# Kernel optimization log

Hardware: AMD Instinct MI355X
Metric: run time of the kernel (lower is better)

Reference implementation:

```python
import jax, jax.numpy as jnp
import numpy as np

G, K, N, T = 16, 2048, 2048, 16384  # groups, in_features, out_features, total_tokens


def setup_inputs() -> dict:
    key = jax.random.key(0)
    k1, k2 = jax.random.split(key)
    hidden_states = jax.random.normal(k1, (T, K), dtype=jnp.float32)
    # kaiming_uniform_(a=sqrt(5)) on [G, K, N] -> bound = sqrt(6 / ((1 + 5) * fan_in)) = 1/sqrt(K)
    bound = 1.0 / np.sqrt(K)
    weight = jax.random.uniform(k2, (G, K, N), dtype=jnp.float32, minval=-bound, maxval=bound)
    tokens_per_group = T // G
    tokens_per_expert = jnp.full((G,), tokens_per_group, dtype=jnp.int32)
    # offsets[0] = 0, offsets[i] = start of group i (matches _group_sizes_from_offsets)
    offsets = jnp.arange(G, dtype=jnp.int32) * tokens_per_group
    blockscale_offsets = offsets  # unused by the eager math path; carried for signature fidelity
    return {
        "hidden_states": hidden_states,
        "weight": weight,
        "offsets": offsets,
        "blockscale_offsets": blockscale_offsets,
        "tokens_per_expert": tokens_per_expert,
    }


def reference(hidden_states, weight, offsets, blockscale_offsets, tokens_per_expert):
    # Grouped (ragged) GEMM: rows [offsets[g] : offsets[g]+tokens_per_expert[g]] of
    # hidden_states are multiplied by weight[g] ([K, N]). tokens_per_expert equals the
    # group sizes derived from offsets in the torch module's eager fallback.
    # jax.lax.ragged_dot is the exact grouped-mm primitive (no dense [T,K,N] gather).
    return jax.lax.ragged_dot(hidden_states, weight, tokens_per_expert)
```

## Files before the change

kernel.cpp:

```cpp
#include <hip/hip_runtime.h>
#include <cstdint>
#include <cstddef>

#define GRP 16
#define KD  2048
#define ND  2048
#define TD  16384

#define BM 128
#define BN 128
#define BK 64

typedef __bf16 bf16x8 __attribute__((ext_vector_type(8)));
typedef float  f32x4  __attribute__((ext_vector_type(4)));

__device__ __forceinline__ uint16_t f2bf(float f) {
  uint32_t u = __builtin_bit_cast(uint32_t, f);
  u += 0x7fffu + ((u >> 16) & 1u);
  return (uint16_t)(u >> 16);
}

__device__ __forceinline__ void gload16(const void* g, void* l) {
  __builtin_amdgcn_global_load_lds((__attribute__((address_space(1))) void*)g,
                                   (__attribute__((address_space(3))) void*)l,
                                   16, 0, 0);
}

__device__ __forceinline__ int find_group(const int* tokens, int row0) {
  int g = GRP - 1, start = 0;
  for (int i = 0; i < GRP; ++i) {
    int sz = tokens[i];
    if (row0 < start + sz) { g = i; break; }
    start += sz;
  }
  return g;
}

__global__ __launch_bounds__(256) void h2bf_kernel(const float* __restrict__ in,
                                                   uint16_t* __restrict__ out) {
  const size_t idx = ((size_t)blockIdx.x * 256 + threadIdx.x) * 8;
  const float4 a = *(const float4*)(in + idx);
  const float4 b = *(const float4*)(in + idx + 4);
  uint4 p;
  p.x = (uint32_t)f2bf(a.x) | ((uint32_t)f2bf(a.y) << 16);
  p.y = (uint32_t)f2bf(a.z) | ((uint32_t)f2bf(a.w) << 16);
  p.z = (uint32_t)f2bf(b.x) | ((uint32_t)f2bf(b.y) << 16);
  p.w = (uint32_t)f2bf(b.z) | ((uint32_t)f2bf(b.w) << 16);
  *(uint4*)(out + idx) = p;
}

__global__ __launch_bounds__(256) void wtrans_kernel(const float* __restrict__ w,
                                                     uint16_t* __restrict__ wT) {
  __shared__ uint32_t tile[64][33];
  const int g  = blockIdx.z;
  const int n0 = blockIdx.x * 64;
  const int k0 = blockIdx.y * 64;
  const float* src = w + (size_t)g * KD * ND;
  uint16_t* dst = wT + (size_t)g * ND * KD;
  const int t = threadIdx.x;

  {
    const int k2 = t >> 4;
    const int n4 = (t & 15) * 4;
    for (int half = 0; half < 2; ++half) {
      const int kp = half * 16 + k2;
      const int k  = kp * 2;
      const float4 v0 = *(const float4*)(src + (size_t)(k0 + k)     * ND + n0 + n4);
      const float4 v1 = *(const float4*)(src + (size_t)(k0 + k + 1) * ND + n0 + n4);
      tile[n4 + 0][kp] = (uint32_t)f2bf(v0.x) | ((uint32_t)f2bf(v1.x) << 16);
      tile[n4 + 1][kp] = (uint32_t)f2bf(v0.y) | ((uint32_t)f2bf(v1.y) << 16);
      tile[n4 + 2][kp] = (uint32_t)f2bf(v0.z) | ((uint32_t)f2bf(v1.z) << 16);
      tile[n4 + 3][kp] = (uint32_t)f2bf(v0.w) | ((uint32_t)f2bf(v1.w) << 16);
    }
  }
  __syncthreads();
  {
    const int n  = t >> 2;
    const int kq = (t & 3) * 8;
    const uint4 a = *(const uint4*)&tile[n][kq];
    const uint4 b = *(const uint4*)&tile[n][kq + 4];
    uint32_t* o = (uint32_t*)(dst + (size_t)(n0 + n) * KD + k0) + kq;
    *(uint4*)(o + 0) = a;
    *(uint4*)(o + 4) = b;
  }
}

__global__ __launch_bounds__(256) void gemm_kernel(const uint16_t* __restrict__ A,
                                                   const uint16_t* __restrict__ Bt,
                                                   const int* __restrict__ tokens,
                                                   float* __restrict__ C) {
  __shared__ uint16_t Alds[BM * BK];
  __shared__ uint16_t Blds[BN * BK];

  const int t    = threadIdx.x;
  const int n0   = blockIdx.x * BN;
  const int row0 = blockIdx.y * BM;

  const int g = find_group(tokens, row0);
  const uint16_t* Bg = Bt + (size_t)g * ND * KD;

  const int lane = t & 63;
  const int wid  = t >> 6;
  const int wm   = wid & 1;
  const int wn   = wid >> 1;
  const int l16  = lane & 15;
  const int quad = lane >> 4;

  f32x4 acc[4][4] = {};

  const uint16_t* Apt[4]; const uint16_t* Bpt[4];
  uint16_t *Al[4], *Bl[4];
  for (int i = 0; i < 4; ++i) {
    const int c = t + 256 * i;
    const int r = c >> 3;
    const int ko = ((c & 7) ^ (r & 7)) * 8;
    Apt[i] = A  + (size_t)(row0 + r) * KD + ko;
    Bpt[i] = Bg + (size_t)(n0  + r) * KD + ko;
    Al[i] = &Alds[c * 8];
    Bl[i] = &Blds[c * 8];
  }

  int aoff[2][4], boff[2][4];
  for (int h = 0; h < 2; ++h) {
    for (int mi = 0; mi < 4; ++mi) {
      const int r = wm * 64 + mi * 16 + l16;
      aoff[h][mi] = r * BK + (((h * 4 + quad) ^ (r & 7)) * 8);
    }
    for (int ni = 0; ni < 4; ++ni) {
      const int r = wn * 64 + ni * 16 + l16;
      boff[h][ni] = r * BK + (((h * 4 + quad) ^ (r & 7)) * 8);
    }
  }

  for (int k0 = 0; k0 < KD; k0 += BK) {
    __syncthreads();
    for (int i = 0; i < 4; ++i) gload16(Apt[i] + k0, Al[i]);
    for (int i = 0; i < 4; ++i) gload16(Bpt[i] + k0, Bl[i]);
    __syncthreads();

    for (int h = 0; h < 2; ++h) {
      bf16x8 af[4], bfr[4];
      for (int mi = 0; mi < 4; ++mi) af[mi]  = *(const bf16x8*)&Alds[aoff[h][mi]];
      for (int ni = 0; ni < 4; ++ni) bfr[ni] = *(const bf16x8*)&Blds[boff[h][ni]];
      for (int mi = 0; mi < 4; ++mi)
        for (int ni = 0; ni < 4; ++ni)
          acc[mi][ni] = __builtin_amdgcn_mfma_f32_16x16x32_bf16(af[mi], bfr[ni],
                                                                acc[mi][ni], 0, 0, 0);
    }
  }

  for (int mi = 0; mi < 4; ++mi) {
    const int m = row0 + wm * 64 + mi * 16 + quad * 4;
    for (int ni = 0; ni < 4; ++ni) {
      const int n = n0 + wn * 64 + ni * 16 + l16;
      for (int r = 0; r < 4; ++r)
        C[(size_t)(m + r) * ND + n] = acc[mi][ni][r];
    }
  }
}

__global__ __launch_bounds__(256) void fb_gemm(const float* __restrict__ A,
                                               const float* __restrict__ W,
                                               const int* __restrict__ tokens,
                                               float* __restrict__ C) {
  __shared__ float As[16][64];
  __shared__ float Bs[16][65];
  const int n0 = blockIdx.x * 64;
  const int m0 = blockIdx.y * 64;
  const int g = find_group(tokens, m0);
  const float* Wg = W + (size_t)g * KD * ND;
  const int tx = threadIdx.x & 15, ty = threadIdx.x >> 4;
  float acc[4][4] = {};
  for (int k0 = 0; k0 < KD; k0 += 16) {
    for (int e = threadIdx.x; e < 64 * 16; e += 256) {
      int m = e >> 4, k = e & 15;
      As[k][m] = A[(size_t)(m0 + m) * KD + k0 + k];
    }
    for (int e = threadIdx.x; e < 64 * 16; e += 256) {
      int n = e & 63, k = e >> 6;
      Bs[k][n] = Wg[(size_t)(k0 + k) * ND + n0 + n];
    }
    __syncthreads();
    for (int k = 0; k < 16; ++k)
      for (int i = 0; i < 4; ++i)
        for (int j = 0; j < 4; ++j)
          acc[i][j] += As[k][ty * 4 + i] * Bs[k][tx * 4 + j];
    __syncthreads();
  }
  for (int i = 0; i < 4; ++i)
    for (int j = 0; j < 4; ++j)
      C[(size_t)(m0 + ty * 4 + i) * ND + n0 + tx * 4 + j] = acc[i][j];
}

extern "C" void kernel_launch(void* const* d_in, const int* in_sizes, int n_in,
                              void* d_out, int out_size, void* d_ws, size_t ws_size,
                              hipStream_t stream) {
  const float* hidden = (const float*)d_in[0];
  const float* weight = (const float*)d_in[1];
  const int*   tokens = (const int*)d_in[4];
  float* out = (float*)d_out;

  const size_t needA = (size_t)TD * KD * 2;
  const size_t needB = (size_t)GRP * ND * KD * 2;

  if (ws_size >= needA + needB) {
    uint16_t* hB = (uint16_t*)d_ws;
    uint16_t* wT = (uint16_t*)((char*)d_ws + needA);
    h2bf_kernel<<<(int)(((size_t)TD * KD) / (256 * 8)), 256, 0, stream>>>(hidden, hB);
    wtrans_kernel<<<dim3(ND / 64, KD / 64, GRP), 256, 0, stream>>>(weight, wT);
    gemm_kernel<<<dim3(ND / BN, TD / BM), 256, 0, stream>>>(hB, wT, tokens, out);
  } else {
    fb_gemm<<<dim3(ND / 64, TD / 64), 256, 0, stream>>>(hidden, weight, tokens, out);
  }
}
```

Baseline: 673.9 us.

## Fuse fp32-to-bf16 conversion and weight transpose into register-prefetched GEMM

Removes the separate conversion and weight-transpose kernels and their workspace round-trip. The GEMM now reads fp32 activations and weights directly, converts them to bf16 in registers, and writes them transposed and swizzled into LDS. The next tile's global loads are issued into registers before the MFMA loop so they overlap with compute. The cost is twice the global bytes per tile, since fp32 inputs are reloaded by every block that uses them, plus strided scalar weight loads and higher register pressure.

```diff
diff --git a/kernel.cpp b/kernel.cpp
--- a/kernel.cpp
+++ b/kernel.cpp
@@ -10,20 +10,17 @@
 #define BM 128
 #define BN 128
 #define BK 64
+#define NT (KD / BK)
 
 typedef __bf16 bf16x8 __attribute__((ext_vector_type(8)));
 typedef float  f32x4  __attribute__((ext_vector_type(4)));
 
-__device__ __forceinline__ uint16_t f2bf(float f) {
-  uint32_t u = __builtin_bit_cast(uint32_t, f);
-  u += 0x7fffu + ((u >> 16) & 1u);
-  return (uint16_t)(u >> 16);
-}
-
-__device__ __forceinline__ void gload16(const void* g, void* l) {
-  __builtin_amdgcn_global_load_lds((__attribute__((address_space(1))) void*)g,
-                                   (__attribute__((address_space(3))) void*)l,
-                                   16, 0, 0);
+__device__ __forceinline__ uint32_t pk2bf(float x, float y) {
+  uint32_t ux = __builtin_bit_cast(uint32_t, x);
+  uint32_t uy = __builtin_bit_cast(uint32_t, y);
+  ux += 0x7fffu + ((ux >> 16) & 1u);
+  uy += 0x7fffu + ((uy >> 16) & 1u);
+  return __builtin_amdgcn_perm(uy, ux, 0x07060302);
 }
 
 __device__ __forceinline__ int find_group(const int* tokens, int row0) {
@@ -36,59 +33,9 @@
   return g;
 }
 
-__global__ __launch_bounds__(256) void h2bf_kernel(const float* __restrict__ in,
-                                                   uint16_t* __restrict__ out) {
-  const size_t idx = ((size_t)blockIdx.x * 256 + threadIdx.x) * 8;
-  const float4 a = *(const float4*)(in + idx);
-  const float4 b = *(const float4*)(in + idx + 4);
-  uint4 p;
-  p.x = (uint32_t)f2bf(a.x) | ((uint32_t)f2bf(a.y) << 16);
-  p.y = (uint32_t)f2bf(a.z) | ((uint32_t)f2bf(a.w) << 16);
-  p.z = (uint32_t)f2bf(b.x) | ((uint32_t)f2bf(b.y) << 16);
-  p.w = (uint32_t)f2bf(b.z) | ((uint32_t)f2bf(b.w) << 16);
-  *(uint4*)(out + idx) = p;
-}
-
-__global__ __launch_bounds__(256) void wtrans_kernel(const float* __restrict__ w,
-                                                     uint16_t* __restrict__ wT) {
-  __shared__ uint32_t tile[64][33];
-  const int g  = blockIdx.z;
-  const int n0 = blockIdx.x * 64;
-  const int k0 = blockIdx.y * 64;
-  const float* src = w + (size_t)g * KD * ND;
-  uint16_t* dst = wT + (size_t)g * ND * KD;
-  const int t = threadIdx.x;
-
-  {
-    const int k2 = t >> 4;
-    const int n4 = (t & 15) * 4;
-    for (int half = 0; half < 2; ++half) {
-      const int kp = half * 16 + k2;
-      const int k  = kp * 2;
-      const float4 v0 = *(const float4*)(src + (size_t)(k0 + k)     * ND + n0 + n4);
-      const float4 v1 = *(const float4*)(src + (size_t)(k0 + k + 1) * ND + n0 + n4);
-      tile[n4 + 0][kp] = (uint32_t)f2bf(v0.x) | ((uint32_t)f2bf(v1.x) << 16);
-      tile[n4 + 1][kp] = (uint32_t)f2bf(v0.y) | ((uint32_t)f2bf(v1.y) << 16);
-      tile[n4 + 2][kp] = (uint32_t)f2bf(v0.z) | ((uint32_t)f2bf(v1.z) << 16);
-      tile[n4 + 3][kp] = (uint32_t)f2bf(v0.w) | ((uint32_t)f2bf(v1.w) << 16);
-    }
-  }
-  __syncthreads();
-  {
-    const int n  = t >> 2;
-    const int kq = (t & 3) * 8;
-    const uint4 a = *(const uint4*)&tile[n][kq];
-    const uint4 b = *(const uint4*)&tile[n][kq + 4];
-    uint32_t* o = (uint32_t*)(dst + (size_t)(n0 + n) * KD + k0) + kq;
-    *(uint4*)(o + 0) = a;
-    *(uint4*)(o + 4) = b;
-  }
-}
-
-__global__ __launch_bounds__(256) void gemm_kernel(const uint16_t* __restrict__ A,
-                                                   const uint16_t* __restrict__ Bt,
-                                                   const int* __restrict__ tokens,
-                                                   float* __restrict__ C) {
+__global__ __launch_bounds__(256, 2)
+void fused_gemm(const float* __restrict__ A, const float* __restrict__ W,
+                const int* __restrict__ tokens, float* __restrict__ C) {
   __shared__ uint16_t Alds[BM * BK];
   __shared__ uint16_t Blds[BN * BK];
 
@@ -97,7 +44,7 @@
   const int row0 = blockIdx.y * BM;
 
   const int g = find_group(tokens, row0);
-  const uint16_t* Bg = Bt + (size_t)g * ND * KD;
+  const float* Wg = W + (size_t)g * KD * ND;
 
   const int lane = t & 63;
   const int wid  = t >> 6;
@@ -106,18 +53,23 @@
   const int l16  = lane & 15;
   const int quad = lane >> 4;
 
-  f32x4 acc[4][4] = {};
+  const float* aptr[4];
+  uint32_t*    adst[4];
+  for (int i = 0; i < 4; ++i) {
+    const int c  = t + 256 * i;
+    const int r  = c >> 3;
+    const int cl = c & 7;
+    aptr[i] = A + (size_t)(row0 + r) * KD + cl * 8;
+    adst[i] = (uint32_t*)&Alds[(r * 8 + (cl ^ (r & 7))) * 8];
+  }
 
-  const uint16_t* Apt[4]; const uint16_t* Bpt[4];
-  uint16_t *Al[4], *Bl[4];
-  for (int i = 0; i < 4; ++i) {
-    const int c = t + 256 * i;
-    const int r = c >> 3;
-    const int ko = ((c & 7) ^ (r & 7)) * 8;
-    Apt[i] = A  + (size_t)(row0 + r) * KD + ko;
-    Bpt[i] = Bg + (size_t)(n0  + r) * KD + ko;
-    Al[i] = &Alds[c * 8];
-    Bl[i] = &Blds[c * 8];
+  const int nl = t & 127;
+  const int bh = t >> 7;
+  const float* bptr = Wg + (size_t)(bh * 32) * ND + n0 + nl;
+  uint32_t* bdst[4];
+  for (int c = 0; c < 4; ++c) {
+    const int kc = bh * 4 + c;
+    bdst[c] = (uint32_t*)&Blds[(nl * 8 + (kc ^ (nl & 7))) * 8];
   }
 
   int aoff[2][4], boff[2][4];
@@ -132,64 +84,80 @@
     }
   }
 
-  for (int k0 = 0; k0 < KD; k0 += BK) {
-    __syncthreads();
-    for (int i = 0; i < 4; ++i) gload16(Apt[i] + k0, Al[i]);
-    for (int i = 0; i < 4; ++i) gload16(Bpt[i] + k0, Bl[i]);
+  f32x4 acc[4][4] = {};
+
+  float4 ar[4][2];
+  float  br[4][8];
+
+  auto issue = [&](int k0) {
+    #pragma unroll
+    for (int i = 0; i < 4; ++i) {
+      ar[i][0] = *(const float4*)(aptr[i] + k0);
+      ar[i][1] = *(const float4*)(aptr[i] + k0 + 4);
+    }
+    const float* bp = bptr + (size_t)k0 * ND;
+    #pragma unroll
+    for (int c = 0; c < 4; ++c)
+      #pragma unroll
+      for (int j = 0; j < 8; ++j)
+        br[c][j] = bp[(size_t)(c * 8 + j) * ND];
+  };
+
+  issue(0);
+
+  for (int kt = 0; kt < NT; ++kt) {
     __syncthreads();
 
+    #pragma unroll
+    for (int i = 0; i < 4; ++i) {
+      uint4 p;
+      p.x = pk2bf(ar[i][0].x, ar[i][0].y);
+      p.y = pk2bf(ar[i][0].z, ar[i][0].w);
+      p.z = pk2bf(ar[i][1].x, ar[i][1].y);
+      p.w = pk2bf(ar[i][1].z, ar[i][1].w);
+      *(uint4*)adst[i] = p;
+    }
+    #pragma unroll
+    for (int c = 0; c < 4; ++c) {
+      uint4 p;
+      p.x = pk2bf(br[c][0], br[c][1]);
+      p.y = pk2bf(br[c][2], br[c][3]);
+      p.z = pk2bf(br[c][4], br[c][5]);
+      p.w = pk2bf(br[c][6], br[c][7]);
+      *(uint4*)bdst[c] = p;
+    }
+
+    if (kt + 1 < NT) issue((kt + 1) * BK);
+
+    __syncthreads();
+
+    #pragma unroll
     for (int h = 0; h < 2; ++h) {
       bf16x8 af[4], bfr[4];
+      #pragma unroll
       for (int mi = 0; mi < 4; ++mi) af[mi]  = *(const bf16x8*)&Alds[aoff[h][mi]];
+      #pragma unroll
       for (int ni = 0; ni < 4; ++ni) bfr[ni] = *(const bf16x8*)&Blds[boff[h][ni]];
+      #pragma unroll
       for (int mi = 0; mi < 4; ++mi)
+        #pragma unroll
         for (int ni = 0; ni < 4; ++ni)
           acc[mi][ni] = __builtin_amdgcn_mfma_f32_16x16x32_bf16(af[mi], bfr[ni],
                                                                 acc[mi][ni], 0, 0, 0);
     }
   }
 
+  #pragma unroll
   for (int mi = 0; mi < 4; ++mi) {
     const int m = row0 + wm * 64 + mi * 16 + quad * 4;
+    #pragma unroll
     for (int ni = 0; ni < 4; ++ni) {
       const int n = n0 + wn * 64 + ni * 16 + l16;
+      #pragma unroll
       for (int r = 0; r < 4; ++r)
         C[(size_t)(m + r) * ND + n] = acc[mi][ni][r];
     }
   }
-}
-
-__global__ __launch_bounds__(256) void fb_gemm(const float* __restrict__ A,
-                                               const float* __restrict__ W,
-                                               const int* __restrict__ tokens,
-                                               float* __restrict__ C) {
-  __shared__ float As[16][64];
-  __shared__ float Bs[16][65];
-  const int n0 = blockIdx.x * 64;
-  const int m0 = blockIdx.y * 64;
-  const int g = find_group(tokens, m0);
-  const float* Wg = W + (size_t)g * KD * ND;
-  const int tx = threadIdx.x & 15, ty = threadIdx.x >> 4;
-  float acc[4][4] = {};
-  for (int k0 = 0; k0 < KD; k0 += 16) {
-    for (int e = threadIdx.x; e < 64 * 16; e += 256) {
-      int m = e >> 4, k = e & 15;
-      As[k][m] = A[(size_t)(m0 + m) * KD + k0 + k];
-    }
-    for (int e = threadIdx.x; e < 64 * 16; e += 256) {
-      int n = e & 63, k = e >> 6;
-      Bs[k][n] = Wg[(size_t)(k0 + k) * ND + n0 + n];
-    }
-    __syncthreads();
-    for (int k = 0; k < 16; ++k)
-      for (int i = 0; i < 4; ++i)
-        for (int j = 0; j < 4; ++j)
-          acc[i][j] += As[k][ty * 4 + i] * Bs[k][tx * 4 + j];
-    __syncthreads();
-  }
-  for (int i = 0; i < 4; ++i)
-    for (int j = 0; j < 4; ++j)
-      C[(size_t)(m0 + ty * 4 + i) * ND + n0 + tx * 4 + j] = acc[i][j];
 }
 
 extern "C" void kernel_launch(void* const* d_in, const int* in_sizes, int n_in,
@@ -199,17 +167,7 @@
   const float* weight = (const float*)d_in[1];
   const int*   tokens = (const int*)d_in[4];
   float* out = (float*)d_out;
+  (void)d_ws; (void)ws_size;
 
-  const size_t needA = (size_t)TD * KD * 2;
-  const size_t needB = (size_t)GRP * ND * KD * 2;
-
-  if (ws_size >= needA + needB) {
-    uint16_t* hB = (uint16_t*)d_ws;
-    uint16_t* wT = (uint16_t*)((char*)d_ws + needA);
-    h2bf_kernel<<<(int)(((size_t)TD * KD) / (256 * 8)), 256, 0, stream>>>(hidden, hB);
-    wtrans_kernel<<<dim3(ND / 64, KD / 64, GRP), 256, 0, stream>>>(weight, wT);
-    gemm_kernel<<<dim3(ND / BN, TD / BM), 256, 0, stream>>>(hB, wT, tokens, out);
-  } else {
-    fb_gemm<<<dim3(ND / 64, TD / 64), 256, 0, stream>>>(hidden, weight, tokens, out);
-  }
+  fused_gemm<<<dim3(ND / BN, TD / BM), 256, 0, stream>>>(hidden, weight, tokens, out);
 }
```

After: 693.9 us. 1.03x slower.

## Rewrite grouped GEMM as 256x256 double-buffered pipelined kernel with block swizzle

Applied to the files above, without the earlier changes.

Replaces the 128x128 single-buffered GEMM with a 256x256 tile, 512-thread kernel that double-buffers A and B tiles in LDS. Global-to-LDS loads for the next K tile are interleaved with MFMA phases, using explicit vmcnt waits, barriers and setprio. Blocks are remapped through a swizzle so neighbouring blocks share weight tiles in L2. It also changes the wtrans store pattern so each wave writes a contiguous run. The cost is heavier register and LDS pressure (8x4 accumulators per thread, 128KB LDS) and fragile hand-written wait counts.

```diff
diff --git a/kernel.cpp b/kernel.cpp
--- a/kernel.cpp
+++ b/kernel.cpp
@@ -7,9 +7,10 @@
 #define ND  2048
 #define TD  16384
 
-#define BM 128
-#define BN 128
+#define BM 256
+#define BN 256
 #define BK 64
+#define NTILE (KD / BK)
 
 typedef __bf16 bf16x8 __attribute__((ext_vector_type(8)));
 typedef float  f32x4  __attribute__((ext_vector_type(4)));
@@ -76,83 +77,134 @@
   __syncthreads();
   {
     const int n  = t >> 2;
-    const int kq = (t & 3) * 8;
+    const int kq = (t & 3) * 4;
     const uint4 a = *(const uint4*)&tile[n][kq];
-    const uint4 b = *(const uint4*)&tile[n][kq + 4];
-    uint32_t* o = (uint32_t*)(dst + (size_t)(n0 + n) * KD + k0) + kq;
-    *(uint4*)(o + 0) = a;
-    *(uint4*)(o + 4) = b;
-  }
-}
-
-__global__ __launch_bounds__(256) void gemm_kernel(const uint16_t* __restrict__ A,
-                                                   const uint16_t* __restrict__ Bt,
-                                                   const int* __restrict__ tokens,
-                                                   float* __restrict__ C) {
-  __shared__ uint16_t Alds[BM * BK];
-  __shared__ uint16_t Blds[BN * BK];
-
-  const int t    = threadIdx.x;
-  const int n0   = blockIdx.x * BN;
-  const int row0 = blockIdx.y * BM;
+    const uint4 b = *(const uint4*)&tile[n][kq + 16];
+    uint32_t* o = (uint32_t*)(dst + (size_t)(n0 + n) * KD + k0);
+    *(uint4*)(o + kq)      = a;
+    *(uint4*)(o + kq + 16) = b;
+  }
+}
+
+__global__ __launch_bounds__(512, 2)
+void gemm_kernel(const uint16_t* __restrict__ A, const uint16_t* __restrict__ Bt,
+                 const int* __restrict__ tokens, float* __restrict__ C) {
+  __shared__ uint16_t Alds[2][2][128 * 64];
+  __shared__ uint16_t Blds[2][2][128 * 64];
+
+  const int t = threadIdx.x;
+  const int bid = blockIdx.x;
+  const int swz = (bid & 7) * 64 + (bid >> 3);
+  const int bx = swz & 7, by = swz >> 3;
+  const int n0 = bx * BN, row0 = by * BM;
 
   const int g = find_group(tokens, row0);
   const uint16_t* Bg = Bt + (size_t)g * ND * KD;
 
-  const int lane = t & 63;
-  const int wid  = t >> 6;
-  const int wm   = wid & 1;
-  const int wn   = wid >> 1;
-  const int l16  = lane & 15;
-  const int quad = lane >> 4;
-
-  f32x4 acc[4][4] = {};
-
-  const uint16_t* Apt[4]; const uint16_t* Bpt[4];
-  uint16_t *Al[4], *Bl[4];
-  for (int i = 0; i < 4; ++i) {
-    const int c = t + 256 * i;
+  const int lane = t & 63, wid = t >> 6;
+  const int wm = wid & 1;
+  const int wn = wid >> 1;
+  const int l16 = lane & 15, quad = lane >> 4;
+
+  const uint16_t* pA[2]; const uint16_t* pB[2];
+  int doff[2];
+  #pragma unroll
+  for (int j = 0; j < 2; ++j) {
+    const int c = t + 512 * j;
     const int r = c >> 3;
     const int ko = ((c & 7) ^ (r & 7)) * 8;
-    Apt[i] = A  + (size_t)(row0 + r) * KD + ko;
-    Bpt[i] = Bg + (size_t)(n0  + r) * KD + ko;
-    Al[i] = &Alds[c * 8];
-    Bl[i] = &Blds[c * 8];
-  }
-
-  int aoff[2][4], boff[2][4];
-  for (int h = 0; h < 2; ++h) {
-    for (int mi = 0; mi < 4; ++mi) {
-      const int r = wm * 64 + mi * 16 + l16;
-      aoff[h][mi] = r * BK + (((h * 4 + quad) ^ (r & 7)) * 8);
-    }
-    for (int ni = 0; ni < 4; ++ni) {
-      const int r = wn * 64 + ni * 16 + l16;
-      boff[h][ni] = r * BK + (((h * 4 + quad) ^ (r & 7)) * 8);
-    }
-  }
-
-  for (int k0 = 0; k0 < KD; k0 += BK) {
-    __syncthreads();
-    for (int i = 0; i < 4; ++i) gload16(Apt[i] + k0, Al[i]);
-    for (int i = 0; i < 4; ++i) gload16(Bpt[i] + k0, Bl[i]);
-    __syncthreads();
-
-    for (int h = 0; h < 2; ++h) {
-      bf16x8 af[4], bfr[4];
-      for (int mi = 0; mi < 4; ++mi) af[mi]  = *(const bf16x8*)&Alds[aoff[h][mi]];
-      for (int ni = 0; ni < 4; ++ni) bfr[ni] = *(const bf16x8*)&Blds[boff[h][ni]];
-      for (int mi = 0; mi < 4; ++mi)
-        for (int ni = 0; ni < 4; ++ni)
-          acc[mi][ni] = __builtin_amdgcn_mfma_f32_16x16x32_bf16(af[mi], bfr[ni],
-                                                                acc[mi][ni], 0, 0, 0);
-    }
-  }
-
-  for (int mi = 0; mi < 4; ++mi) {
-    const int m = row0 + wm * 64 + mi * 16 + quad * 4;
+    pA[j] = A  + (size_t)(row0 + r) * KD + ko;
+    pB[j] = Bg + (size_t)(n0  + r) * KD + ko;
+    doff[j] = c * 8;
+  }
+
+  int arow[8], brow[4], axk[2];
+  #pragma unroll
+  for (int mi = 0; mi < 8; ++mi) arow[mi] = (mi * 16 + l16) * 64;
+  #pragma unroll
+  for (int ni = 0; ni < 4; ++ni) brow[ni] = ((wn & 1) * 64 + ni * 16 + l16) * 64;
+  #pragma unroll
+  for (int kh = 0; kh < 2; ++kh) axk[kh] = ((kh * 4 + quad) ^ (l16 & 7)) * 8;
+
+  const uint16_t* Abase[2] = { &Alds[0][wm][0],      &Alds[1][wm][0] };
+  const uint16_t* Bbase[2] = { &Blds[0][wn >> 1][0], &Blds[1][wn >> 1][0] };
+
+  f32x4 acc[8][4] = {};
+  bf16x8 bfr[2][4];
+
+#define STAGE_A(buf, half, T) do {                                              \
+    gload16(pA[0] + (size_t)(half) * 128 * KD + (T) * BK, &Alds[buf][half][doff[0]]); \
+    gload16(pA[1] + (size_t)(half) * 128 * KD + (T) * BK, &Alds[buf][half][doff[1]]); \
+  } while (0)
+#define STAGE_B(buf, half, T) do {                                              \
+    gload16(pB[0] + (size_t)(half) * 128 * KD + (T) * BK, &Blds[buf][half][doff[0]]); \
+    gload16(pB[1] + (size_t)(half) * 128 * KD + (T) * BK, &Blds[buf][half][doff[1]]); \
+  } while (0)
+#define NOSTAGE do {} while (0)
+#define VM4 asm volatile("s_waitcnt vmcnt(4)" ::: "memory")
+#define VM0 asm volatile("s_waitcnt vmcnt(0)" ::: "memory")
+#define NOWAIT do {} while (0)
+#define LGK0 asm volatile("s_waitcnt lgkmcnt(0)" ::: "memory")
+#define BARRIER do { asm volatile("" ::: "memory");                             \
+    __builtin_amdgcn_s_barrier(); asm volatile("" ::: "memory"); } while (0)
+
+#define PHASE(buf, mib, DO_B, STAGE_STMT, ENDWAIT) do {                         \
+    if (DO_B) {                                                                 \
+      _Pragma("unroll") for (int kh2 = 0; kh2 < 2; ++kh2)                       \
+        _Pragma("unroll") for (int ni2 = 0; ni2 < 4; ++ni2)                     \
+          bfr[kh2][ni2] = *(const bf16x8*)&Bbase[buf][brow[ni2] + axk[kh2]];    \
+    }                                                                           \
+    bf16x8 af[2][2];                                                            \
+    _Pragma("unroll") for (int kh2 = 0; kh2 < 2; ++kh2)                         \
+      _Pragma("unroll") for (int m2 = 0; m2 < 2; ++m2)                          \
+        af[kh2][m2] = *(const bf16x8*)&Abase[buf][arow[(mib) + m2] + axk[kh2]]; \
+    STAGE_STMT;                                                                 \
+    BARRIER;                                                                    \
+    __builtin_amdgcn_s_setprio(1);                                              \
+    _Pragma("unroll") for (int kh2 = 0; kh2 < 2; ++kh2)                         \
+      _Pragma("unroll") for (int m2 = 0; m2 < 2; ++m2)                          \
+        _Pragma("unroll") for (int ni2 = 0; ni2 < 4; ++ni2)                     \
+          acc[(mib) + m2][ni2] = __builtin_amdgcn_mfma_f32_16x16x32_bf16(       \
+              af[kh2][m2], bfr[kh2][ni2], acc[(mib) + m2][ni2], 0, 0, 0);       \
+    __builtin_amdgcn_s_setprio(0);                                              \
+    LGK0;                                                                       \
+    ENDWAIT;                                                                    \
+    BARRIER;                                                                    \
+  } while (0)
+
+  STAGE_B(0, 0, 0); STAGE_B(0, 1, 0);
+  STAGE_A(0, 0, 0); STAGE_A(0, 1, 0);
+  STAGE_B(1, 0, 1); STAGE_B(1, 1, 1);
+  VM4;
+  BARRIER;
+
+  for (int i = 0; i < NTILE / 2 - 1; ++i) {
+    const int t1 = 2 * i + 1, t2 = 2 * i + 2, t3 = 2 * i + 3;
+    PHASE(0, 0, true,  STAGE_A(1, 0, t1), NOWAIT);
+    PHASE(0, 2, false, STAGE_A(1, 1, t1), NOWAIT);
+    PHASE(0, 4, false, STAGE_B(0, 0, t2), NOWAIT);
+    PHASE(0, 6, false, STAGE_B(0, 1, t2), VM4);
+    PHASE(1, 0, true,  STAGE_A(0, 0, t2), NOWAIT);
+    PHASE(1, 2, false, STAGE_A(0, 1, t2), NOWAIT);
+    PHASE(1, 4, false, STAGE_B(1, 0, t3), NOWAIT);
+    PHASE(1, 6, false, STAGE_B(1, 1, t3), VM4);
+  }
+  PHASE(0, 0, true,  STAGE_A(1, 0, NTILE - 1), NOWAIT);
+  PHASE(0, 2, false, STAGE_A(1, 1, NTILE - 1), NOWAIT);
+  PHASE(0, 4, false, NOSTAGE, NOWAIT);
+  PHASE(0, 6, false, NOSTAGE, VM0);
+  PHASE(1, 0, true,  NOSTAGE, NOWAIT);
+  PHASE(1, 2, false, NOSTAGE, NOWAIT);
+  PHASE(1, 4, false, NOSTAGE, NOWAIT);
+  PHASE(1, 6, false, NOSTAGE, NOWAIT);
+
+  #pragma unroll
+  for (int mi = 0; mi < 8; ++mi) {
+    const int m = row0 + wm * 128 + mi * 16 + quad * 4;
+    #pragma unroll
     for (int ni = 0; ni < 4; ++ni) {
       const int n = n0 + wn * 64 + ni * 16 + l16;
+      #pragma unroll
       for (int r = 0; r < 4; ++r)
         C[(size_t)(m + r) * ND + n] = acc[mi][ni][r];
     }
@@ -208,7 +260,7 @@
     uint16_t* wT = (uint16_t*)((char*)d_ws + needA);
     h2bf_kernel<<<(int)(((size_t)TD * KD) / (256 * 8)), 256, 0, stream>>>(hidden, hB);
     wtrans_kernel<<<dim3(ND / 64, KD / 64, GRP), 256, 0, stream>>>(weight, wT);
-    gemm_kernel<<<dim3(ND / BN, TD / BM), 256, 0, stream>>>(hB, wT, tokens, out);
+    gemm_kernel<<<dim3(TD / BM * (ND / BN)), 512, 0, stream>>>(hB, wT, tokens, out);
   } else {
     fb_gemm<<<dim3(ND / 64, TD / 64), 256, 0, stream>>>(hidden, weight, tokens, out);
   }
```

Result: faster. 638.8 us (-5.2%).
